# Kernel tuning notes

Hardware: AMD Instinct MI355X
Metric: run time of the kernel (lower is better)

## Reference

```python
import jax, jax.numpy as jnp
import numpy as np

KS = 5          # kernel_size
D = 2           # spatial dim
DX = 0.01       # region kernel spacing
SCALE = 1.0
NX, NY = 32, 32
N = NX * NY


def _region_kernel():
    # gaussians.region_kernel: KS x KS grid of offsets spaced DX, centered at 0
    off = (jnp.arange(KS, dtype=jnp.float32) - (KS - 1) / 2.0) * DX
    gx, gy = jnp.meshgrid(off, off, indexing='ij')
    return jnp.stack([gx, gy], -1).reshape(-1, D)  # (KS*KS, 2)


def _build_cov(scaling, transform):
    # Cholesky-style parameterization: L lower-triangular with diag=scaling,
    # off-diag=transform; cov = L @ L^T (d=2 closed form)
    s0, s1 = scaling[:, 0], scaling[:, 1]
    t = transform[:, 0]
    c00 = s0 * s0
    c01 = s0 * t
    c11 = t * t + s1 * s1
    return jnp.stack([jnp.stack([c00, c01], -1), jnp.stack([c01, c11], -1)], -2)


def _inv2x2(c):
    det = c[:, 0, 0] * c[:, 1, 1] - c[:, 0, 1] * c[:, 1, 0]
    inv = jnp.stack([jnp.stack([c[:, 1, 1], -c[:, 0, 1]], -1),
                     jnp.stack([-c[:, 1, 0], c[:, 0, 0]], -1)], -2)
    return inv / det[:, None, None]


def setup_inputs() -> dict:
    key = jax.random.key(0)
    ks = jax.random.split(key, 20)
    # Gaussian state: grid means as in __init__
    tx = jnp.linspace(-1.0, 1.0, NX) * SCALE
    ty = jnp.linspace(-1.0, 1.0, NY) * SCALE
    gx, gy = jnp.meshgrid(tx, ty, indexing='ij')
    means = jnp.stack([gx, gy], -1).reshape(-1, D).astype(jnp.float32)
    u = 0.1 * jax.random.normal(ks[0], (N, 1), jnp.float32)
    scaling = jnp.exp(-4.5 + 0.2 * jax.random.normal(ks[1], (N, D), jnp.float32)) * SCALE
    transform = 0.002 * jax.random.normal(ks[2], (N, 1), jnp.float32)
    opacities = 2.0 + 0.1 * jax.random.normal(ks[3], (N,), jnp.float32)
    # network weights (4 heads share the first 3 layer shapes)
    convW = 0.05 * jax.random.normal(ks[4], (4, 50, 3, KS, KS), jnp.float32)
    convb = 0.01 * jax.random.normal(ks[5], (4, 50), jnp.float32)
    embW = 0.3 * jax.random.normal(ks[6], (4, 7, 30), jnp.float32)
    embb = 0.01 * jax.random.normal(ks[7], (4, 30), jnp.float32)
    l1W = 0.1 * jax.random.normal(ks[8], (4, 80, 80), jnp.float32)
    l1b = 0.01 * jax.random.normal(ks[9], (4, 80), jnp.float32)
    outW_sol = 0.1 * jax.random.normal(ks[10], (80, 1), jnp.float32)
    outb_sol = 0.01 * jax.random.normal(ks[11], (1,), jnp.float32)
    outW_trans = 0.1 * jax.random.normal(ks[12], (80, 2), jnp.float32)
    outb_trans = 0.01 * jax.random.normal(ks[13], (2,), jnp.float32)
    outW_scale = 0.1 * jax.random.normal(ks[14], (80, 2), jnp.float32)
    outb_scale = 0.01 * jax.random.normal(ks[15], (2,), jnp.float32)
    outW_tform = 0.1 * jax.random.normal(ks[16], (80, 1), jnp.float32)
    outb_tform = 0.01 * jax.random.normal(ks[17], (1,), jnp.float32)
    return {"means": means, "u": u, "scaling": scaling, "transform": transform,
            "opacities": opacities, "convW": convW, "convb": convb,
            "embW": embW, "embb": embb, "l1W": l1W, "l1b": l1b,
            "outW_sol": outW_sol, "outb_sol": outb_sol,
            "outW_trans": outW_trans, "outb_trans": outb_trans,
            "outW_scale": outW_scale, "outb_scale": outb_scale,
            "outW_tform": outW_tform, "outb_tform": outb_tform}


def reference(means, u, scaling, transform, opacities, convW, convb, embW, embb,
              l1W, l1b, outW_sol, outb_sol, outW_trans, outb_trans,
              outW_scale, outb_scale, outW_tform, outb_tform):
    n = means.shape[0]
    cov = _build_cov(scaling, transform)          # (N,2,2)
    conics = _inv2x2(cov)                         # (N,2,2)

    # --- sampling (torch.no_grad block in original) ---
    kern = _region_kernel()                                        # (25,2)
    samples = (means[:, None, :] + kern[None]).reshape(-1, D)      # (M,2), M=N*25
    bc = jnp.all(jnp.abs(samples) < SCALE, -1).astype(means.dtype)[:, None]
    alpha = jax.nn.sigmoid(opacities)                              # (N,)
    diff = samples[:, None, :] - means[None, :, :]                 # (M,N,2)
    Cq = jnp.einsum('nij,mnj->mni', conics, diff)                  # (M,N,2)
    G = jnp.exp(-0.5 * jnp.einsum('mni,mni->mn', diff, Cq)) * alpha[None, :]  # (M,N)
    u_s = G @ u                                                    # (M,1)
    # DIFFUSION pde_rhs = trace of laplacian: sum_n G * (|C q|^2 - tr(C)) * u_n
    trC = conics[:, 0, 0] + conics[:, 1, 1]
    lap = jnp.einsum('mn,mn,nc->mc', G, (Cq ** 2).sum(-1) - trC[None, :], u)  # (M,1)
    in_samples = jax.lax.stop_gradient(jnp.concatenate([u_s, lap, bc], -1))   # (M,3)

    # (N, 25, 3) -> (N, 3, 5, 5)
    img = in_samples.reshape(n, KS * KS, -1).transpose(0, 2, 1).reshape(n, -1, KS, KS)
    in_params = jnp.concatenate([means, u, scaling, transform, opacities[:, None]], -1)  # (N,7)

    # 4 Networks: conv(5x5 -> 1x1, 50ch) + param embed(7->30) + MLP(80->80->out)
    y = jnp.tanh(jnp.einsum('ncij,kocij->kno', img, convW) + convb[:, None, :])   # (4,N,50)
    e = jnp.tanh(jnp.einsum('nf,kfg->kng', in_params, embW) + embb[:, None, :])   # (4,N,30)
    h = jnp.tanh(jnp.einsum('knf,kfg->kng', jnp.concatenate([y, e], -1), l1W)
                 + l1b[:, None, :])                                               # (4,N,80)

    deltas = h[0] @ outW_sol + outb_sol          # (N,1)
    translation = h[1] @ outW_trans + outb_trans # (N,2)
    dscale = h[2] @ outW_scale + outb_scale      # (N,2)
    dtransform = h[3] @ outW_tform + outb_tform  # (N,1)

    u_new = u + deltas
    means_new = means + translation
    scaling_new = scaling * jnp.exp(dscale)
    transform_new = transform + dtransform
    cov_new = _build_cov(scaling_new, transform_new)
    return (u_new, means_new, scaling_new, transform_new, cov_new)
```

## Files before the change

kernel.cpp:

```cpp
#include <hip/hip_runtime.h>
#include <hip/hip_bf16.h>


#define NG 1024
#define WS_GD   0
#define WS_CWT  (NG * 8)

__device__ __forceinline__ float tanh_fast(float x) {
    return 1.0f - 2.0f / (__expf(2.0f * x) + 1.0f);
}

__global__ __launch_bounds__(256) void k_prep(
    const float* __restrict__ means, const float* __restrict__ u,
    const float* __restrict__ scal,  const float* __restrict__ trans,
    const float* __restrict__ opac,  const float* __restrict__ convW,
    float* __restrict__ ws)
{
    int gid = blockIdx.x * 256 + threadIdx.x;
    if (gid < NG) {
        float gmx = means[2*gid], gmy = means[2*gid+1];
        float s0  = scal[2*gid],  s1  = scal[2*gid+1];
        float tt  = trans[gid];
        float c00 = s0*s0, c01 = s0*tt, c11 = tt*tt + s1*s1;
        float idet = 1.0f / (c00*c11 - c01*c01);
        float A = c11*idet, B = -c01*idet, C = c00*idet;
        float alpha = 1.0f / (1.0f + __expf(-opac[gid]));
        float r2 = 100.0f * (c00 + c11);
        float4* dst = (float4*)(ws + WS_GD + gid*8);
        dst[0] = make_float4(gmx, gmy, A, B);
        dst[1] = make_float4(C, A + C, alpha * u[gid], r2);
    }
    float* wt = ws + WS_CWT;
    for (int idx = gid; idx < 15000; idx += gridDim.x * 256) {
        int ko = idx / 75, j = idx - ko * 75;
        wt[j * 200 + ko] = convW[idx];
    }
}

__global__ __launch_bounds__(256) void k_fused(
    const float* __restrict__ means, const float* __restrict__ u,
    const float* __restrict__ scal, const float* __restrict__ trans,
    const float* __restrict__ opac,
    const float* __restrict__ convb,
    const float* __restrict__ embW,  const float* __restrict__ embb,
    const float* __restrict__ l1W,   const float* __restrict__ l1b,
    const float* __restrict__ oWs,  const float* __restrict__ obs,
    const float* __restrict__ oWt,  const float* __restrict__ obt,
    const float* __restrict__ oWsc, const float* __restrict__ obsc,
    const float* __restrict__ oWtf, const float* __restrict__ obtf,
    const float* __restrict__ ws,
    float* __restrict__ out)
{
    __shared__ float gcomp[NG * 8];
    __shared__ float pus[2][4][32];
    __shared__ float plap[2][4][32];
    __shared__ float simg[2][80];
    __shared__ float hin[2][4][80];
    __shared__ float hv[2][4][80];
    __shared__ float outs[2][8];
    __shared__ int   cnt;

    const int t  = threadIdx.x;
    const int n0 = blockIdx.x * 2;
    const float mx0 = means[2*n0],   my0 = means[2*n0+1];
    const float mx1 = means[2*n0+2], my1 = means[2*n0+3];
    const float bxmin = fminf(mx0, mx1) - 0.02f, bxmax = fmaxf(mx0, mx1) + 0.02f;
    const float bymin = fminf(my0, my1) - 0.02f, bymax = fmaxf(my0, my1) + 0.02f;

    if (t == 0) cnt = 0;
    __syncthreads();
    for (int g = t; g < NG; g += 256) {
        const float4* src = (const float4*)(ws + WS_GD + g*8);
        float4 a = src[0], b = src[1];
        float ddx = fmaxf(fmaxf(bxmin - a.x, a.x - bxmax), 0.0f);
        float ddy = fmaxf(fmaxf(bymin - a.y, a.y - bymax), 0.0f);
        if (ddx*ddx + ddy*ddy <= b.w) {
            int slot = atomicAdd(&cnt, 1);
            float4* dst = (float4*)(gcomp + slot*8);
            dst[0] = a; dst[1] = b;
        }
    }
    __syncthreads();
    const int nsurv = cnt;

    {
        int c = t >> 6, lane = t & 63, l = lane >> 5, s = lane & 31;
        if (s < 25) {
            int si = s / 5, sj = s - si * 5;
            float gx = l ? mx1 : mx0, gy = l ? my1 : my0;
            float sx = gx + (float)(si - 2) * 0.01f;
            float sy = gy + (float)(sj - 2) * 0.01f;
            float us = 0.0f, lp = 0.0f;
            #pragma unroll 2
            for (int i = c; i < nsurv; i += 4) {
                float4 a = *(const float4*)(gcomp + i*8);
                float4 b = *(const float4*)(gcomp + i*8 + 4);
                float dx = sx - a.x, dy = sy - a.y;
                float Cq0 = a.z*dx + a.w*dy;
                float Cq1 = a.w*dx + b.x*dy;
                float q   = dx*Cq0 + dy*Cq1;
                float e   = __expf(-0.5f*q) * b.z;
                us += e;
                lp += e * (Cq0*Cq0 + Cq1*Cq1 - b.y);
            }
            pus[l][c][s] = us; plap[l][c][s] = lp;
        }
    }
    __syncthreads();

    if (t < 50) {
        int l = t / 25, s = t - l * 25;
        float us = 0.0f, lp = 0.0f;
        #pragma unroll
        for (int c = 0; c < 4; ++c) { us += pus[l][c][s]; lp += plap[l][c][s]; }
        int si = s / 5, sj = s - si * 5;
        float gx = l ? mx1 : mx0, gy = l ? my1 : my0;
        float sx = gx + (float)(si - 2) * 0.01f;
        float sy = gy + (float)(sj - 2) * 0.01f;
        simg[l][s]      = us;
        simg[l][25 + s] = lp;
        simg[l][50 + s] = (fabsf(sx) < 1.0f && fabsf(sy) < 1.0f) ? 1.0f : 0.0f;
    }
    __syncthreads();

    if (t < 200) {
        const float* wt = ws + WS_CWT;
        float a0 = convb[t], a1 = a0;
        #pragma unroll 5
        for (int j = 0; j < 75; ++j) {
            float w = wt[j*200 + t];
            a0 += simg[0][j] * w;
            a1 += simg[1][j] * w;
        }
        int k = t / 50, o = t - k * 50;
        hin[0][k][o] = tanh_fast(a0);
        hin[1][k][o] = tanh_fast(a1);
    } else {
        for (int idx = t - 200; idx < 240; idx += 56) {
            int l = idx / 120, rem = idx - l * 120;
            int k = rem / 30, g = rem - k * 30;
            int n = n0 + l;
            float inp[7] = { means[2*n], means[2*n+1], u[n], scal[2*n],
                             scal[2*n+1], trans[n], opac[n] };
            float acc = embb[k * 30 + g];
            #pragma unroll
            for (int f = 0; f < 7; ++f) acc += inp[f] * embW[(k*7 + f)*30 + g];
            hin[l][k][50 + g] = tanh_fast(acc);
        }
    }
    __syncthreads();

    for (int p = t; p < 320; p += 256) {
        int k = p / 80, g = p - k * 80;
        float a0 = l1b[p], a1 = a0;
        #pragma unroll 8
        for (int f = 0; f < 80; ++f) {
            float w = l1W[(k*80 + f)*80 + g];
            a0 += hin[0][k][f] * w;
            a1 += hin[1][k][f] * w;
        }
        hv[0][k][g] = tanh_fast(a0);
        hv[1][k][g] = tanh_fast(a1);
    }
    __syncthreads();

    if (t < 12) {
        int l = t / 6, t6 = t - l * 6;
        const float* W; const float* bb; int k, j, stride;
        if (t6 == 0)      { W = oWs;  bb = obs;  k = 0; j = 0;      stride = 1; }
        else if (t6 < 3)  { W = oWt;  bb = obt;  k = 1; j = t6 - 1; stride = 2; }
        else if (t6 < 5)  { W = oWsc; bb = obsc; k = 2; j = t6 - 3; stride = 2; }
        else              { W = oWtf; bb = obtf; k = 3; j = 0;      stride = 1; }
        float acc = bb[j];
        #pragma unroll 8
        for (int f = 0; f < 80; ++f) acc += hv[l][k][f] * W[f * stride + j];
        outs[l][t6] = acc;
    }
    __syncthreads();

    if (t < 2) {
        int n = n0 + t;
        float uu = u[n];
        float s0 = scal[2*n], s1 = scal[2*n+1];
        float tr = trans[n];
        float u_new = uu + outs[t][0];
        float mxn = (t ? mx1 : mx0) + outs[t][1];
        float myn = (t ? my1 : my0) + outs[t][2];
        float s0n = s0 * __expf(outs[t][3]);
        float s1n = s1 * __expf(outs[t][4]);
        float tn  = tr + outs[t][5];
        float c00 = s0n*s0n, c01 = s0n*tn, c11 = tn*tn + s1n*s1n;
        out[n]              = u_new;
        out[1024 + 2*n]     = mxn;
        out[1024 + 2*n + 1] = myn;
        out[3072 + 2*n]     = s0n;
        out[3072 + 2*n + 1] = s1n;
        out[5120 + n]       = tn;
        out[6144 + 4*n]     = c00;
        out[6144 + 4*n + 1] = c01;
        out[6144 + 4*n + 2] = c01;
        out[6144 + 4*n + 3] = c11;
    }
}

extern "C" void kernel_launch(void* const* d_in, const int* in_sizes, int n_in,
                              void* d_out, int out_size, void* d_ws, size_t ws_size,
                              hipStream_t stream)
{
    const float* means = (const float*)d_in[0];
    const float* u     = (const float*)d_in[1];
    const float* scal  = (const float*)d_in[2];
    const float* trans = (const float*)d_in[3];
    const float* opac  = (const float*)d_in[4];
    const float* convW = (const float*)d_in[5];
    float* ws = (float*)d_ws;

    k_prep<<<dim3(64), dim3(256), 0, stream>>>(means, u, scal, trans, opac,
                                               convW, ws);
    k_fused<<<dim3(NG / 2), dim3(256), 0, stream>>>(
        means, u, scal, trans, opac,
        (const float*)d_in[6],  (const float*)d_in[7],  (const float*)d_in[8],
        (const float*)d_in[9],  (const float*)d_in[10], (const float*)d_in[11],
        (const float*)d_in[12], (const float*)d_in[13], (const float*)d_in[14],
        (const float*)d_in[15], (const float*)d_in[16], (const float*)d_in[17],
        (const float*)d_in[18], ws, (float*)d_out);
}
```

Baseline: 108.7 us.

## Fold prep kernel into fused kernel, compute gaussian params on the fly

```diff
diff --git a/kernel.cpp b/kernel.cpp
--- a/kernel.cpp
+++ b/kernel.cpp
@@ -3,52 +3,22 @@
 
 
 #define NG 1024
-#define WS_GD   0
-#define WS_CWT  (NG * 8)
 
 __device__ __forceinline__ float tanh_fast(float x) {
     return 1.0f - 2.0f / (__expf(2.0f * x) + 1.0f);
-}
-
-__global__ __launch_bounds__(256) void k_prep(
-    const float* __restrict__ means, const float* __restrict__ u,
-    const float* __restrict__ scal,  const float* __restrict__ trans,
-    const float* __restrict__ opac,  const float* __restrict__ convW,
-    float* __restrict__ ws)
-{
-    int gid = blockIdx.x * 256 + threadIdx.x;
-    if (gid < NG) {
-        float gmx = means[2*gid], gmy = means[2*gid+1];
-        float s0  = scal[2*gid],  s1  = scal[2*gid+1];
-        float tt  = trans[gid];
-        float c00 = s0*s0, c01 = s0*tt, c11 = tt*tt + s1*s1;
-        float idet = 1.0f / (c00*c11 - c01*c01);
-        float A = c11*idet, B = -c01*idet, C = c00*idet;
-        float alpha = 1.0f / (1.0f + __expf(-opac[gid]));
-        float r2 = 100.0f * (c00 + c11);
-        float4* dst = (float4*)(ws + WS_GD + gid*8);
-        dst[0] = make_float4(gmx, gmy, A, B);
-        dst[1] = make_float4(C, A + C, alpha * u[gid], r2);
-    }
-    float* wt = ws + WS_CWT;
-    for (int idx = gid; idx < 15000; idx += gridDim.x * 256) {
-        int ko = idx / 75, j = idx - ko * 75;
-        wt[j * 200 + ko] = convW[idx];
-    }
 }
 
 __global__ __launch_bounds__(256) void k_fused(
     const float* __restrict__ means, const float* __restrict__ u,
     const float* __restrict__ scal, const float* __restrict__ trans,
     const float* __restrict__ opac,
-    const float* __restrict__ convb,
+    const float* __restrict__ convW, const float* __restrict__ convb,
     const float* __restrict__ embW,  const float* __restrict__ embb,
     const float* __restrict__ l1W,   const float* __restrict__ l1b,
     const float* __restrict__ oWs,  const float* __restrict__ obs,
     const float* __restrict__ oWt,  const float* __restrict__ obt,
     const float* __restrict__ oWsc, const float* __restrict__ obsc,
     const float* __restrict__ oWtf, const float* __restrict__ obtf,
-    const float* __restrict__ ws,
     float* __restrict__ out)
 {
     __shared__ float gcomp[NG * 8];
@@ -70,14 +40,21 @@
     if (t == 0) cnt = 0;
     __syncthreads();
     for (int g = t; g < NG; g += 256) {
-        const float4* src = (const float4*)(ws + WS_GD + g*8);
-        float4 a = src[0], b = src[1];
-        float ddx = fmaxf(fmaxf(bxmin - a.x, a.x - bxmax), 0.0f);
-        float ddy = fmaxf(fmaxf(bymin - a.y, a.y - bymax), 0.0f);
-        if (ddx*ddx + ddy*ddy <= b.w) {
+        float gmx = means[2*g], gmy = means[2*g+1];
+        float s0  = scal[2*g],  s1  = scal[2*g+1];
+        float tt  = trans[g];
+        float c00 = s0*s0, c01 = s0*tt, c11 = tt*tt + s1*s1;
+        float r2  = 100.0f * (c00 + c11);
+        float ddx = fmaxf(fmaxf(bxmin - gmx, gmx - bxmax), 0.0f);
+        float ddy = fmaxf(fmaxf(bymin - gmy, gmy - bymax), 0.0f);
+        if (ddx*ddx + ddy*ddy <= r2) {
+            float idet = 1.0f / (c00*c11 - c01*c01);
+            float A = c11*idet, B = -c01*idet, C = c00*idet;
+            float alpha = 1.0f / (1.0f + __expf(-opac[g]));
             int slot = atomicAdd(&cnt, 1);
             float4* dst = (float4*)(gcomp + slot*8);
-            dst[0] = a; dst[1] = b;
+            dst[0] = make_float4(gmx, gmy, A, B);
+            dst[1] = make_float4(C, A + C, alpha * u[g], 0.0f);
         }
     }
     __syncthreads();
@@ -124,13 +101,13 @@
     __syncthreads();
 
     if (t < 200) {
-        const float* wt = ws + WS_CWT;
+        const float* w = convW + (size_t)t * 75;
         float a0 = convb[t], a1 = a0;
         #pragma unroll 5
         for (int j = 0; j < 75; ++j) {
-            float w = wt[j*200 + t];
-            a0 += simg[0][j] * w;
-            a1 += simg[1][j] * w;
+            float wj = w[j];
+            a0 += simg[0][j] * wj;
+            a1 += simg[1][j] * wj;
         }
         int k = t / 50, o = t - k * 50;
         hin[0][k][o] = tanh_fast(a0);
@@ -207,21 +184,12 @@
                               void* d_out, int out_size, void* d_ws, size_t ws_size,
                               hipStream_t stream)
 {
-    const float* means = (const float*)d_in[0];
-    const float* u     = (const float*)d_in[1];
-    const float* scal  = (const float*)d_in[2];
-    const float* trans = (const float*)d_in[3];
-    const float* opac  = (const float*)d_in[4];
-    const float* convW = (const float*)d_in[5];
-    float* ws = (float*)d_ws;
-
-    k_prep<<<dim3(64), dim3(256), 0, stream>>>(means, u, scal, trans, opac,
-                                               convW, ws);
     k_fused<<<dim3(NG / 2), dim3(256), 0, stream>>>(
-        means, u, scal, trans, opac,
+        (const float*)d_in[0],  (const float*)d_in[1],  (const float*)d_in[2],
+        (const float*)d_in[3],  (const float*)d_in[4],  (const float*)d_in[5],
         (const float*)d_in[6],  (const float*)d_in[7],  (const float*)d_in[8],
         (const float*)d_in[9],  (const float*)d_in[10], (const float*)d_in[11],
         (const float*)d_in[12], (const float*)d_in[13], (const float*)d_in[14],
         (const float*)d_in[15], (const float*)d_in[16], (const float*)d_in[17],
-        (const float*)d_in[18], ws, (float*)d_out);
+        (const float*)d_in[18], (float*)d_out);
 }
```

New measurement: 108.0 us. Within noise of the previous version (-0.6%).
